# Performance work log

Measured on AMD Instinct MI355X. Metric: run time of the kernel, lower is better.

The kernel has to match this reference:

```python
import jax, jax.numpy as jnp
import numpy as np

DIM = 1024
HEADS = 16
B, N = 4, 2048


def setup_inputs() -> dict:
    key = jax.random.key(0)
    ks = jax.random.split(key, 6)
    scale = DIM ** -0.5
    return {
        "x": jax.random.normal(ks[0], (B, N, DIM), dtype=jnp.float32),
        "mask": jax.random.randint(ks[1], (B, N, N), 0, 2) > 0,
        "Wqkv": jax.random.normal(ks[2], (DIM, 3 * DIM), dtype=jnp.float32) * scale,
        "bqkv": jax.random.normal(ks[3], (3 * DIM,), dtype=jnp.float32) * 0.02,
        "Wproj": jax.random.normal(ks[4], (DIM, DIM), dtype=jnp.float32) * scale,
        "bproj": jax.random.normal(ks[5], (DIM,), dtype=jnp.float32) * 0.02,
    }


def reference(x, mask, Wqkv, bqkv, Wproj, bproj):
    Bs, Ns, C = x.shape
    H = HEADS
    D = C // H
    scale = D ** -0.5
    qkv = x @ Wqkv + bqkv                       # [B, N, 3C]
    qkv = qkv.reshape(Bs, Ns, 3, H, D)          # split (three h d)
    q, k, v = jnp.moveaxis(qkv, 2, 0)           # each [B, N, H, D]
    q = q.transpose(0, 2, 1, 3)                 # [B, H, N, D]
    k = k.transpose(0, 2, 1, 3)
    v = v.transpose(0, 2, 1, 3)
    attn = jnp.einsum("bhnd,bhmd->bhnm", q, k) * scale  # [B, H, N, N]
    attn = jnp.where(mask[:, None, :, :], -jnp.inf, attn)
    attn = jax.nn.softmax(attn, axis=-1)
    out = jnp.einsum("bhnm,bhmd->bhnd", attn, v)        # [B, H, N, D]
    out = out.transpose(0, 2, 1, 3).reshape(Bs, Ns, C)  # [B, N, C]
    return out @ Wproj + bproj
```

## Files before the change

kernel.cpp:

```cpp
#include <hip/hip_runtime.h>
#include <cstdint>
#include <cstddef>

constexpr int kC = 1024;
constexpr int kH = 16;
constexpr int kB = 4;
constexpr int kN = 2048;
constexpr int kD = 64;

#define KQ_SCALE 0.18033688011112042f

typedef unsigned short u16;
typedef unsigned int   u32;
typedef unsigned long long u64;
typedef __bf16 v8bf  __attribute__((ext_vector_type(8)));
typedef __bf16 v4bf  __attribute__((ext_vector_type(4)));
typedef float  v4f   __attribute__((ext_vector_type(4)));
typedef u16    u16x8 __attribute__((ext_vector_type(8)));
typedef u16    u16x4 __attribute__((ext_vector_type(4)));

__device__ inline u16 f2bf(float f) {
    union { float f; unsigned u; } v; v.f = f;
    unsigned r = v.u + 0x7FFFu + ((v.u >> 16) & 1u);
    return (u16)(r >> 16);
}

__device__ inline float fast_exp2(float x) {
#if __has_builtin(__builtin_amdgcn_exp2f)
    return __builtin_amdgcn_exp2f(x);
#else
    return __expf(x * 0.6931471805599453f);
#endif
}

__device__ inline void gl2lds16(const u16* g, u16* l) {
    __builtin_amdgcn_global_load_lds(
        (const __attribute__((address_space(1))) void*)g,
        (__attribute__((address_space(3))) void*)l, 16, 0, 0);
}

__global__ __launch_bounds__(256) void cast_bf16_kernel(
    const float* __restrict__ in, u16* __restrict__ outp)
{
    const int i = blockIdx.x * 256 + threadIdx.x;
    const float4 f = ((const float4*)in)[i];
    u16x4 o;
    o.x = f2bf(f.x); o.y = f2bf(f.y); o.z = f2bf(f.z); o.w = f2bf(f.w);
    ((u16x4*)outp)[i] = o;
}

__global__ __launch_bounds__(256) void tpose_cast_kernel(
    const float* __restrict__ W, u16* __restrict__ Wt, int R, int Cc)
{
    __shared__ u16 tile[64][65];
    const int c0 = blockIdx.x * 64;
    const int r0 = blockIdx.y * 64;
    const int t  = threadIdx.x;
#pragma unroll
    for (int it = 0; it < 16; ++it) {
        const int r = it * 4 + (t >> 6);
        const int c = t & 63;
        tile[c][r] = f2bf(W[(size_t)(r0 + r) * Cc + c0 + c]);
    }
    __syncthreads();
#pragma unroll
    for (int it = 0; it < 16; ++it) {
        const int rr = it * 4 + (t >> 6);
        const int cc = t & 63;
        Wt[(size_t)(c0 + rr) * R + r0 + cc] = tile[rr][cc];
    }
}

__global__ __launch_bounds__(256) void maskpack_kernel(
    const int* __restrict__ mask, u32* __restrict__ bits)
{
    const int seg  = blockIdx.x * 4 + (threadIdx.x >> 6);
    const int lane = threadIdx.x & 63;
    const size_t row = (size_t)(seg >> 5);
    const int s = seg & 31;
    const int m = mask[row * kN + s * 64 + lane];
    const u64 bal = __ballot(m != 0);
    if (lane == 0) ((u64*)bits)[row * 32 + s] = bal;
}

template <int MODE>
__global__ __launch_bounds__(256) void gemm_mfma_kernel(
    const u16* __restrict__ A, const u16* __restrict__ Bt,
    const float* __restrict__ bias, float* __restrict__ Cout,
    u16* __restrict__ qOut, u16* __restrict__ kOut, u16* __restrict__ vOut,
    int M, int N, int K)
{
    __shared__ u16 As[128 * 32];
    __shared__ u16 Bs[128 * 32];
    const int t    = threadIdx.x;
    const int w    = t >> 6;
    const int lane = t & 63;
    const int quad = lane >> 4;
    const int l16  = lane & 15;
    const int m0   = blockIdx.y * 128;
    const int n0   = blockIdx.x * 128;

    const int sr = lane >> 2;
    const int sk = (lane & 3) * 8;
    const u16* Ag0 = A  + (size_t)(m0 + 32 * w      + sr) * K + sk;
    const u16* Ag1 = A  + (size_t)(m0 + 32 * w + 16 + sr) * K + sk;
    const u16* Bg0 = Bt + (size_t)(n0 + 32 * w      + sr) * K + sk;
    const u16* Bg1 = Bt + (size_t)(n0 + 32 * w + 16 + sr) * K + sk;
    u16* Al0 = &As[(32 * w)      * 32];
    u16* Al1 = &As[(32 * w + 16) * 32];
    u16* Bl0 = &Bs[(32 * w)      * 32];
    u16* Bl1 = &Bs[(32 * w + 16) * 32];

    v4f acc[4][4];
#pragma unroll
    for (int r = 0; r < 4; ++r)
#pragma unroll
        for (int c = 0; c < 4; ++c) acc[r][c] = (v4f){0.f, 0.f, 0.f, 0.f};

    const int mrow = (w >> 1) * 64;
    const int ncol = (w & 1) * 64;

    for (int k0 = 0; k0 < K; k0 += 32) {
        __syncthreads();
        gl2lds16(Ag0 + k0, Al0);
        gl2lds16(Ag1 + k0, Al1);
        gl2lds16(Bg0 + k0, Bl0);
        gl2lds16(Bg1 + k0, Bl1);
        __syncthreads();

        v8bf af[4], bfr[4];
#pragma unroll
        for (int r = 0; r < 4; ++r)
            af[r] = *(const v8bf*)(&As[(mrow + r * 16 + l16) * 32 + quad * 8]);
#pragma unroll
        for (int c = 0; c < 4; ++c)
            bfr[c] = *(const v8bf*)(&Bs[(ncol + c * 16 + l16) * 32 + quad * 8]);
#pragma unroll
        for (int r = 0; r < 4; ++r)
#pragma unroll
            for (int c = 0; c < 4; ++c)
                acc[r][c] = __builtin_amdgcn_mfma_f32_16x16x32_bf16(
                    af[r], bfr[c], acc[r][c], 0, 0, 0);
    }

#pragma unroll
    for (int r = 0; r < 4; ++r) {
#pragma unroll
        for (int c = 0; c < 4; ++c) {
            const int col = n0 + ncol + c * 16 + l16;
            const float bv = bias[col];
#pragma unroll
            for (int reg = 0; reg < 4; ++reg) {
                const int row = m0 + mrow + r * 16 + quad * 4 + reg;
                float val = acc[r][c][reg] + bv;
                if (MODE == 0) {
                    Cout[(size_t)row * N + col] = val;
                } else {
                    const int which = col >> 10;
                    const int rem   = col & 1023;
                    const int h     = rem >> 6;
                    const int d     = rem & 63;
                    const int b     = row >> 11;
                    const int n     = row & 2047;
                    if (which == 0) val *= KQ_SCALE;
                    u16* dst = (which == 0) ? qOut : (which == 1) ? kOut : vOut;
                    dst[(((size_t)(b * kH + h)) * kN + n) * kD + d] = f2bf(val);
                }
            }
        }
    }
}

__global__ __launch_bounds__(256, 3) void attn_mfma_kernel(
    const u16* __restrict__ q, const u16* __restrict__ k,
    const u16* __restrict__ v, const u32* __restrict__ mbits,
    u16* __restrict__ out)
{
    __shared__ u16 Ks[128 * 64];
    __shared__ u16 Vt[64 * 128];
    __shared__ u16 Ps[64 * 128];

    const int t    = threadIdx.x;
    const int w    = t >> 6;
    const int lane = t & 63;
    const int quad = lane >> 4;
    const int l16  = lane & 15;

    const int bh    = blockIdx.x >> 5;
    const int tile0 = (blockIdx.x & 31) * 64;
    const int b     = bh >> 4;
    const int h     = bh & 15;

    const u16* qb = q + (size_t)bh * kN * kD;
    const u16* kb = k + (size_t)bh * kN * kD;
    const u16* vb = v + (size_t)bh * kN * kD;

    const int qrow = tile0 + w * 16 + l16;
    const v8bf qf0 = *(const v8bf*)(qb + (size_t)qrow * kD + quad * 8);
    const v8bf qf1 = *(const v8bf*)(qb + (size_t)qrow * kD + 32 + quad * 8);

    const u32* mrowb = mbits + ((size_t)b * kN + qrow) * 64;

    const int skr  = t >> 1;
    const int skh  = t & 1;
    const int vg   = t >> 4;
    const int vdq  = t & 15;
    const u16* kgp = kb + (size_t)skr * kD + skh * 32;
    const u16* vgp = vb + (size_t)(vg * 8) * kD + vdq * 4;

    u16x8 kpre[4];
    u16x4 vpre[8];
    uint4 mpre;
    auto prefetch = [&](int k0) {
        const u16x8* ks = (const u16x8*)(kgp + (size_t)k0 * kD);
        kpre[0] = ks[0]; kpre[1] = ks[1]; kpre[2] = ks[2]; kpre[3] = ks[3];
        const u16* vs = vgp + (size_t)k0 * kD;
#pragma unroll
        for (int i = 0; i < 8; ++i)
            vpre[i] = *(const u16x4*)(vs + (size_t)i * kD);
        mpre = *(const uint4*)(mrowb + (k0 >> 5));
    };

    v4f oacc[4];
#pragma unroll
    for (int i = 0; i < 4; ++i) oacc[i] = (v4f){0.f, 0.f, 0.f, 0.f};
    float rs = 0.f;

    prefetch(0);

    for (int kt = 0; kt < kN / 128; ++kt) {
        u16x8 kcur[4];
        u16x4 vcur[8];
#pragma unroll
        for (int i = 0; i < 4; ++i) kcur[i] = kpre[i];
#pragma unroll
        for (int i = 0; i < 8; ++i) vcur[i] = vpre[i];
        const uint4 mcur = mpre;
        const u32 mw[4] = {mcur.x, mcur.y, mcur.z, mcur.w};
        if (kt + 1 < kN / 128) prefetch((kt + 1) * 128);

        __syncthreads();

        {
            const int cb = skh * 4;
            u16* drow = &Ks[skr * 64];
#pragma unroll
            for (int i = 0; i < 4; ++i)
                *(u16x8*)(&drow[((cb + i) ^ (skr & 7)) * 8]) = kcur[i];
        }
        {
#pragma unroll
            for (int dd = 0; dd < 4; ++dd) {
                const int d = vdq * 4 + dd;
                u16x8 col;
#pragma unroll
                for (int j = 0; j < 8; ++j) col[j] = vcur[j][dd];
                *(u16x8*)(&Vt[d * 128 + ((vg ^ (d & 15)) * 8)]) = col;
            }
        }
        __syncthreads();

#pragma unroll
        for (int nb = 0; nb < 8; ++nb) {
            const int krow = nb * 16 + l16;
            const v8bf kf0 = *(const v8bf*)(&Ks[krow * 64 + ((quad       ^ (krow & 7)) * 8)]);
            const v8bf kf1 = *(const v8bf*)(&Ks[krow * 64 + (((quad + 4) ^ (krow & 7)) * 8)]);
            v4f s = (v4f){0.f, 0.f, 0.f, 0.f};
            s = __builtin_amdgcn_mfma_f32_16x16x32_bf16(kf0, qf0, s, 0, 0, 0);
            s = __builtin_amdgcn_mfma_f32_16x16x32_bf16(kf1, qf1, s, 0, 0, 0);

            const u32 m4 = (mw[nb >> 1] >> ((nb & 1) * 16 + quad * 4)) & 0xFu;
            float e0 = fast_exp2(s[0]);
            float e1 = fast_exp2(s[1]);
            float e2 = fast_exp2(s[2]);
            float e3 = fast_exp2(s[3]);
            e0 = (m4 & 1u) ? 0.f : e0;
            e1 = (m4 & 2u) ? 0.f : e1;
            e2 = (m4 & 4u) ? 0.f : e2;
            e3 = (m4 & 8u) ? 0.f : e3;
            rs += (e0 + e1) + (e2 + e3);

            v4bf pw = {(__bf16)e0, (__bf16)e1, (__bf16)e2, (__bf16)e3};
            const int pblk = nb * 2 + (quad >> 1);
            *(v4bf*)(&Ps[(w * 16 + l16) * 128 + ((pblk ^ l16) * 8) + (quad & 1) * 4]) = pw;
        }

        __builtin_amdgcn_s_setprio(1);
#pragma unroll
        for (int ks = 0; ks < 4; ++ks) {
            const v8bf pa = *(const v8bf*)(&Ps[(w * 16 + l16) * 128 + (((ks * 4 + quad) ^ l16) * 8)]);
#pragma unroll
            for (int db = 0; db < 4; ++db) {
                const int d = db * 16 + l16;
                const v8bf vf = *(const v8bf*)(&Vt[d * 128 + (((ks * 4 + quad) ^ (d & 15)) * 8)]);
                oacc[db] = __builtin_amdgcn_mfma_f32_16x16x32_bf16(pa, vf, oacc[db], 0, 0, 0);
            }
        }
        __builtin_amdgcn_s_setprio(0);
    }

    rs += __shfl_xor(rs, 16);
    rs += __shfl_xor(rs, 32);
    const float inv = 1.f / rs;
    float rq[4];
#pragma unroll
    for (int reg = 0; reg < 4; ++reg)
        rq[reg] = __shfl(inv, quad * 4 + reg);

#pragma unroll
    for (int db = 0; db < 4; ++db) {
#pragma unroll
        for (int reg = 0; reg < 4; ++reg) {
            const int row = tile0 + w * 16 + quad * 4 + reg;
            const int col = h * 64 + db * 16 + l16;
            out[((size_t)(b * kN + row)) * kC + col] = f2bf(oacc[db][reg] * rq[reg]);
        }
    }
}

extern "C" void kernel_launch(void* const* d_in, const int* in_sizes, int n_in,
                              void* d_out, int out_size, void* d_ws, size_t ws_size,
                              hipStream_t stream)
{
    const float* x     = (const float*)d_in[0];
    const int*   mask  = (const int*)d_in[1];
    const float* Wqkv  = (const float*)d_in[2];
    const float* bqkv  = (const float*)d_in[3];
    const float* Wproj = (const float*)d_in[4];
    const float* bproj = (const float*)d_in[5];
    float* out = (float*)d_out;

    const size_t nx = (size_t)kB * kN * kC;
    const size_t qkv_elems = (size_t)kB * kH * kN * kD;
    u16* xb     = (u16*)d_ws;
    u16* qbuf   = xb + nx;
    u16* kbuf   = qbuf + qkv_elems;
    u16* vbuf   = kbuf + qkv_elems;
    u16* aob    = vbuf + qkv_elems;
    u16* Wqkvt  = aob + nx;
    u16* Wprojt = Wqkvt + (size_t)3 * kC * kC;
    u32* mbits  = (u32*)(Wprojt + (size_t)kC * kC);

    maskpack_kernel<<<dim3(kB * kN * 32 / 4), dim3(256), 0, stream>>>(mask, mbits);
    cast_bf16_kernel<<<dim3(nx / 1024), dim3(256), 0, stream>>>(x, xb);
    tpose_cast_kernel<<<dim3(3 * kC / 64, kC / 64), dim3(256), 0, stream>>>(
        Wqkv, Wqkvt, kC, 3 * kC);
    tpose_cast_kernel<<<dim3(kC / 64, kC / 64), dim3(256), 0, stream>>>(
        Wproj, Wprojt, kC, kC);

    gemm_mfma_kernel<1><<<dim3(3 * kC / 128, kB * kN / 128), dim3(256), 0, stream>>>(
        xb, Wqkvt, bqkv, nullptr, qbuf, kbuf, vbuf, kB * kN, 3 * kC, kC);

    attn_mfma_kernel<<<dim3(kB * kH * (kN / 64)), dim3(256), 0, stream>>>(
        qbuf, kbuf, vbuf, mbits, aob);

    gemm_mfma_kernel<0><<<dim3(kC / 128, kB * kN / 128), dim3(256), 0, stream>>>(
        aob, Wprojt, bproj, out, nullptr, nullptr, nullptr, kB * kN, kC, kC);
}
```

Before: 403.3 us.

## Double query rows per wave, keep P in registers, compute row sums via MFMA

The attention kernel now handles 128 query rows per block (32 per wave, in two 16-row subtiles), so each K/V tile staged in LDS is reused across twice as many queries and the grid is halved. The P matrix no longer round-trips through LDS. The S-MFMA output layout is repacked directly into the A-operand registers for the PV MFMA, and the row sums come from an MFMA against a ones vector instead of scalar adds and shuffles. The V loads are re-indexed so the register packing matches, and the prefetch is moved after the LDS stores. In exchange, register pressure rises and launch bounds drop to 2 blocks per SM, which lowers occupancy.

```diff
diff --git a/kernel.cpp b/kernel.cpp
--- a/kernel.cpp
+++ b/kernel.cpp
@@ -18,6 +18,7 @@
 typedef float  v4f   __attribute__((ext_vector_type(4)));
 typedef u16    u16x8 __attribute__((ext_vector_type(8)));
 typedef u16    u16x4 __attribute__((ext_vector_type(4)));
+typedef u32    u32x4 __attribute__((ext_vector_type(4)));
 
 __device__ inline u16 f2bf(float f) {
     union { float f; unsigned u; } v; v.f = f;
@@ -171,14 +172,13 @@
     }
 }
 
-__global__ __launch_bounds__(256, 3) void attn_mfma_kernel(
+__global__ __launch_bounds__(256, 2) void attn_mfma_kernel(
     const u16* __restrict__ q, const u16* __restrict__ k,
     const u16* __restrict__ v, const u32* __restrict__ mbits,
     u16* __restrict__ out)
 {
     __shared__ u16 Ks[128 * 64];
     __shared__ u16 Vt[64 * 128];
-    __shared__ u16 Ps[64 * 128];
 
     const int t    = threadIdx.x;
     const int w    = t >> 6;
@@ -186,8 +186,8 @@
     const int quad = lane >> 4;
     const int l16  = lane & 15;
 
-    const int bh    = blockIdx.x >> 5;
-    const int tile0 = (blockIdx.x & 31) * 64;
+    const int bh    = blockIdx.x >> 4;
+    const int tile0 = (blockIdx.x & 15) * 128;
     const int b     = bh >> 4;
     const int h     = bh & 15;
 
@@ -195,50 +195,55 @@
     const u16* kb = k + (size_t)bh * kN * kD;
     const u16* vb = v + (size_t)bh * kN * kD;
 
-    const int qrow = tile0 + w * 16 + l16;
-    const v8bf qf0 = *(const v8bf*)(qb + (size_t)qrow * kD + quad * 8);
-    const v8bf qf1 = *(const v8bf*)(qb + (size_t)qrow * kD + 32 + quad * 8);
-
-    const u32* mrowb = mbits + ((size_t)b * kN + qrow) * 64;
+    const int qrow0 = tile0 + w * 32 + l16;
+    const int qrow1 = qrow0 + 16;
+    v8bf qf[2][2];
+    qf[0][0] = *(const v8bf*)(qb + (size_t)qrow0 * kD + quad * 8);
+    qf[0][1] = *(const v8bf*)(qb + (size_t)qrow0 * kD + 32 + quad * 8);
+    qf[1][0] = *(const v8bf*)(qb + (size_t)qrow1 * kD + quad * 8);
+    qf[1][1] = *(const v8bf*)(qb + (size_t)qrow1 * kD + 32 + quad * 8);
 
     const int skr  = t >> 1;
     const int skh  = t & 1;
     const int vg   = t >> 4;
     const int vdq  = t & 15;
-    const u16* kgp = kb + (size_t)skr * kD + skh * 32;
-    const u16* vgp = vb + (size_t)(vg * 8) * kD + vdq * 4;
+    const int vrow0 = (vg >> 2) * 32 + (vg & 3) * 4;
+
+    const u16* kp = kb + (size_t)skr * kD + skh * 32;
+    const u16* vp = vb + (size_t)vrow0 * kD + vdq * 4;
+    const uint4* mp0 = (const uint4*)(mbits + ((size_t)b * kN + qrow0) * 64);
+    const uint4* mp1 = (const uint4*)(mbits + ((size_t)b * kN + qrow1) * 64);
 
     u16x8 kpre[4];
     u16x4 vpre[8];
-    uint4 mpre;
-    auto prefetch = [&](int k0) {
-        const u16x8* ks = (const u16x8*)(kgp + (size_t)k0 * kD);
-        kpre[0] = ks[0]; kpre[1] = ks[1]; kpre[2] = ks[2]; kpre[3] = ks[3];
-        const u16* vs = vgp + (size_t)k0 * kD;
+    uint4 mpre0, mpre1;
+    auto issue_prefetch = [&]() {
+#pragma unroll
+        for (int i = 0; i < 4; ++i)
+            kpre[i] = *(const u16x8*)(kp + i * 8);
 #pragma unroll
         for (int i = 0; i < 8; ++i)
-            vpre[i] = *(const u16x4*)(vs + (size_t)i * kD);
-        mpre = *(const uint4*)(mrowb + (k0 >> 5));
+            vpre[i] = *(const u16x4*)(vp + (i < 4 ? i * 64 : 1024 + (i - 4) * 64));
+        mpre0 = *mp0; mpre1 = *mp1;
+        kp += 128 * kD; vp += 128 * kD; ++mp0; ++mp1;
     };
 
-    v4f oacc[4];
-#pragma unroll
-    for (int i = 0; i < 4; ++i) oacc[i] = (v4f){0.f, 0.f, 0.f, 0.f};
-    float rs = 0.f;
-
-    prefetch(0);
+    v8bf onesf;
+#pragma unroll
+    for (int j = 0; j < 8; ++j) onesf[j] = (__bf16)1.0f;
+
+    v4f oacc[2][4];
+    v4f rsacc[2];
+#pragma unroll
+    for (int qs = 0; qs < 2; ++qs) {
+        rsacc[qs] = (v4f){0.f, 0.f, 0.f, 0.f};
+#pragma unroll
+        for (int i = 0; i < 4; ++i) oacc[qs][i] = (v4f){0.f, 0.f, 0.f, 0.f};
+    }
+
+    issue_prefetch();
 
     for (int kt = 0; kt < kN / 128; ++kt) {
-        u16x8 kcur[4];
-        u16x4 vcur[8];
-#pragma unroll
-        for (int i = 0; i < 4; ++i) kcur[i] = kpre[i];
-#pragma unroll
-        for (int i = 0; i < 8; ++i) vcur[i] = vpre[i];
-        const uint4 mcur = mpre;
-        const u32 mw[4] = {mcur.x, mcur.y, mcur.z, mcur.w};
-        if (kt + 1 < kN / 128) prefetch((kt + 1) * 128);
-
         __syncthreads();
 
         {
@@ -246,7 +251,7 @@
             u16* drow = &Ks[skr * 64];
 #pragma unroll
             for (int i = 0; i < 4; ++i)
-                *(u16x8*)(&drow[((cb + i) ^ (skr & 7)) * 8]) = kcur[i];
+                *(u16x8*)(&drow[((cb + i) ^ (skr & 7)) * 8]) = kpre[i];
         }
         {
 #pragma unroll
@@ -254,67 +259,89 @@
                 const int d = vdq * 4 + dd;
                 u16x8 col;
 #pragma unroll
-                for (int j = 0; j < 8; ++j) col[j] = vcur[j][dd];
+                for (int j = 0; j < 8; ++j) col[j] = vpre[j][dd];
                 *(u16x8*)(&Vt[d * 128 + ((vg ^ (d & 15)) * 8)]) = col;
             }
         }
+        const uint4 mc0 = mpre0, mc1 = mpre1;
+        if (kt + 1 < kN / 128) issue_prefetch();
         __syncthreads();
+
+        const u32 mwa[2][4] = {{mc0.x, mc0.y, mc0.z, mc0.w},
+                               {mc1.x, mc1.y, mc1.z, mc1.w}};
+        u32 pf[2][4][4];
 
 #pragma unroll
         for (int nb = 0; nb < 8; ++nb) {
             const int krow = nb * 16 + l16;
             const v8bf kf0 = *(const v8bf*)(&Ks[krow * 64 + ((quad       ^ (krow & 7)) * 8)]);
             const v8bf kf1 = *(const v8bf*)(&Ks[krow * 64 + (((quad + 4) ^ (krow & 7)) * 8)]);
-            v4f s = (v4f){0.f, 0.f, 0.f, 0.f};
-            s = __builtin_amdgcn_mfma_f32_16x16x32_bf16(kf0, qf0, s, 0, 0, 0);
-            s = __builtin_amdgcn_mfma_f32_16x16x32_bf16(kf1, qf1, s, 0, 0, 0);
-
-            const u32 m4 = (mw[nb >> 1] >> ((nb & 1) * 16 + quad * 4)) & 0xFu;
-            float e0 = fast_exp2(s[0]);
-            float e1 = fast_exp2(s[1]);
-            float e2 = fast_exp2(s[2]);
-            float e3 = fast_exp2(s[3]);
-            e0 = (m4 & 1u) ? 0.f : e0;
-            e1 = (m4 & 2u) ? 0.f : e1;
-            e2 = (m4 & 4u) ? 0.f : e2;
-            e3 = (m4 & 8u) ? 0.f : e3;
-            rs += (e0 + e1) + (e2 + e3);
-
-            v4bf pw = {(__bf16)e0, (__bf16)e1, (__bf16)e2, (__bf16)e3};
-            const int pblk = nb * 2 + (quad >> 1);
-            *(v4bf*)(&Ps[(w * 16 + l16) * 128 + ((pblk ^ l16) * 8) + (quad & 1) * 4]) = pw;
+#pragma unroll
+            for (int qs = 0; qs < 2; ++qs) {
+                v4f s = (v4f){0.f, 0.f, 0.f, 0.f};
+                s = __builtin_amdgcn_mfma_f32_16x16x32_bf16(kf0, qf[qs][0], s, 0, 0, 0);
+                s = __builtin_amdgcn_mfma_f32_16x16x32_bf16(kf1, qf[qs][1], s, 0, 0, 0);
+
+                const u32 m4 = (mwa[qs][nb >> 1] >> ((nb & 1) * 16 + quad * 4)) & 0xFu;
+                float e0 = fast_exp2(s[0]);
+                float e1 = fast_exp2(s[1]);
+                float e2 = fast_exp2(s[2]);
+                float e3 = fast_exp2(s[3]);
+                e0 = (m4 & 1u) ? 0.f : e0;
+                e1 = (m4 & 2u) ? 0.f : e1;
+                e2 = (m4 & 4u) ? 0.f : e2;
+                e3 = (m4 & 8u) ? 0.f : e3;
+
+                union { v4bf v; u32 u[2]; } bu;
+                bu.v = (v4bf){(__bf16)e0, (__bf16)e1, (__bf16)e2, (__bf16)e3};
+                pf[qs][nb >> 1][(nb & 1) * 2 + 0] = bu.u[0];
+                pf[qs][nb >> 1][(nb & 1) * 2 + 1] = bu.u[1];
+            }
         }
 
+        v8bf pa[2][4];
+#pragma unroll
+        for (int qs = 0; qs < 2; ++qs)
+#pragma unroll
+            for (int ks = 0; ks < 4; ++ks) {
+                u32x4 t4 = {pf[qs][ks][0], pf[qs][ks][1], pf[qs][ks][2], pf[qs][ks][3]};
+                pa[qs][ks] = __builtin_bit_cast(v8bf, t4);
+            }
+
         __builtin_amdgcn_s_setprio(1);
 #pragma unroll
-        for (int ks = 0; ks < 4; ++ks) {
-            const v8bf pa = *(const v8bf*)(&Ps[(w * 16 + l16) * 128 + (((ks * 4 + quad) ^ l16) * 8)]);
+        for (int qs = 0; qs < 2; ++qs)
+#pragma unroll
+            for (int ks = 0; ks < 4; ++ks)
+                rsacc[qs] = __builtin_amdgcn_mfma_f32_16x16x32_bf16(
+                    pa[qs][ks], onesf, rsacc[qs], 0, 0, 0);
+#pragma unroll
+        for (int ks = 0; ks < 4; ++ks)
 #pragma unroll
             for (int db = 0; db < 4; ++db) {
                 const int d = db * 16 + l16;
                 const v8bf vf = *(const v8bf*)(&Vt[d * 128 + (((ks * 4 + quad) ^ (d & 15)) * 8)]);
-                oacc[db] = __builtin_amdgcn_mfma_f32_16x16x32_bf16(pa, vf, oacc[db], 0, 0, 0);
-            }
-        }
+#pragma unroll
+                for (int qs = 0; qs < 2; ++qs)
+                    oacc[qs][db] = __builtin_amdgcn_mfma_f32_16x16x32_bf16(
+                        pa[qs][ks], vf, oacc[qs][db], 0, 0, 0);
+            }
         __builtin_amdgcn_s_setprio(0);
     }
 
-    rs += __shfl_xor(rs, 16);
-    rs += __shfl_xor(rs, 32);
-    const float inv = 1.f / rs;
-    float rq[4];
-#pragma unroll
-    for (int reg = 0; reg < 4; ++reg)
-        rq[reg] = __shfl(inv, quad * 4 + reg);
-
-#pragma unroll
-    for (int db = 0; db < 4; ++db) {
-#pragma unroll
-        for (int reg = 0; reg < 4; ++reg) {
-            const int row = tile0 + w * 16 + quad * 4 + reg;
-            const int col = h * 64 + db * 16 + l16;
-            out[((size_t)(b * kN + row)) * kC + col] = f2bf(oacc[db][reg] * rq[reg]);
-        }
+#pragma unroll
+    for (int qs = 0; qs < 2; ++qs) {
+        float inv[4];
+#pragma unroll
+        for (int reg = 0; reg < 4; ++reg) inv[reg] = 1.f / rsacc[qs][reg];
+#pragma unroll
+        for (int db = 0; db < 4; ++db)
+#pragma unroll
+            for (int reg = 0; reg < 4; ++reg) {
+                const int row = tile0 + w * 32 + qs * 16 + quad * 4 + reg;
+                const int col = h * 64 + db * 16 + l16;
+                out[((size_t)(b * kN + row)) * kC + col] = f2bf(oacc[qs][db][reg] * inv[reg]);
+            }
     }
 }
 
@@ -351,7 +378,7 @@
     gemm_mfma_kernel<1><<<dim3(3 * kC / 128, kB * kN / 128), dim3(256), 0, stream>>>(
         xb, Wqkvt, bqkv, nullptr, qbuf, kbuf, vbuf, kB * kN, 3 * kC, kC);
 
-    attn_mfma_kernel<<<dim3(kB * kH * (kN / 64)), dim3(256), 0, stream>>>(
+    attn_mfma_kernel<<<dim3(kB * kH * (kN / 128)), dim3(256), 0, stream>>>(
         qbuf, kbuf, vbuf, mbits, aob);
 
     gemm_mfma_kernel<0><<<dim3(kC / 128, kB * kN / 128), dim3(256), 0, stream>>>(
```

Result: faster. 375.4 us (-6.9%).
